# Kernel tuning notes

Hardware: AMD Instinct MI355X
Metric: run time of the kernel (lower is better)

## Reference

```python
import jax, jax.numpy as jnp
import numpy as np

N_NODES = 100
K = 8
EPS = 1e-8

def gru_last_hidden(x_seq, Wih, Whh, bih, bhh):
    # x_seq: [T, N, F]; torch GRU gate order: r, z, n
    xW = jnp.einsum('tnf,gf->tng', x_seq, Wih) + bih  # [T, N, 3H]
    H = Whh.shape[1]
    def step(h, xw):
        hW = h @ Whh.T + bhh
        xr, xz, xn = jnp.split(xw, 3, axis=-1)
        hr, hz, hn = jnp.split(hW, 3, axis=-1)
        r = jax.nn.sigmoid(xr + hr)
        z = jax.nn.sigmoid(xz + hz)
        n = jnp.tanh(xn + r * hn)
        h_new = (1.0 - z) * n + z * h
        return h_new, None
    h0 = jnp.zeros((x_seq.shape[1], H), x_seq.dtype)
    hT, _ = jax.lax.scan(step, h0, xW)
    return hT  # [N, H]

def knn_edges(emb, k):
    # cosine sim, zero diagonal, top-k neighbors per row
    nrm = jnp.linalg.norm(emb, axis=1, keepdims=True)
    a = emb / jnp.maximum(nrm, EPS)
    sim = a @ a.T
    idx = jnp.arange(sim.shape[0])
    sim = sim.at[idx, idx].set(0.0)
    _, tgt = jax.lax.top_k(sim, k)               # [N, k]
    src = jnp.broadcast_to(idx[:, None], tgt.shape)
    return src.reshape(-1), tgt.reshape(-1)      # each [N*k]

def sage_conv(x, src, tgt, Wl, Wr, b):
    # PyG SAGEConv (mean aggr): lin_l(mean of neighbor msgs) + lin_r(x) + b
    msg = x[src]                                  # [E, D]
    agg = jax.ops.segment_sum(msg, tgt, num_segments=x.shape[0])
    cnt = jax.ops.segment_sum(jnp.ones((src.shape[0],), x.dtype), tgt,
                              num_segments=x.shape[0])
    agg = agg / jnp.maximum(cnt, 1.0)[:, None]
    return agg @ Wl.T + x @ Wr.T + b

def setup_inputs() -> dict:
    key = jax.random.key(0)
    ks = jax.random.split(key, 16)
    T, N, F, H = 2048, N_NODES, 128, 512
    EMB, FLAT_IN, FLAT_OUT = 128, 32, 64
    GIN = H + FLAT_OUT + EMB       # 704
    GH, GOUT = 256, 128
    OUT_IN = GOUT + H              # 640
    s = 0.02
    return {
        'node_feat': jax.random.normal(ks[0], (T, N, F), jnp.float32),
        'flat': jax.random.normal(ks[1], (N, FLAT_IN), jnp.float32),
        'emb': jax.random.normal(ks[2], (N, EMB), jnp.float32) * s,
        'gru_Wih': jax.random.normal(ks[3], (3 * H, F), jnp.float32) * s,
        'gru_Whh': jax.random.normal(ks[4], (3 * H, H), jnp.float32) * s,
        'gru_bih': jnp.zeros((3 * H,), jnp.float32),
        'gru_bhh': jnp.zeros((3 * H,), jnp.float32),
        'flat_W': jax.random.normal(ks[5], (FLAT_OUT, FLAT_IN), jnp.float32) * s,
        'flat_b': jnp.zeros((FLAT_OUT,), jnp.float32),
        'sage1_Wl': jax.random.normal(ks[6], (GH, GIN), jnp.float32) * s,
        'sage1_Wr': jax.random.normal(ks[7], (GH, GIN), jnp.float32) * s,
        'sage1_b': jnp.zeros((GH,), jnp.float32),
        'sage2_Wl': jax.random.normal(ks[8], (GOUT, GH), jnp.float32) * s,
        'sage2_Wr': jax.random.normal(ks[9], (GOUT, GH), jnp.float32) * s,
        'sage2_b': jnp.zeros((GOUT,), jnp.float32),
        'out_W': jax.random.normal(ks[10], (1, OUT_IN), jnp.float32) * s,
        'out_b': jnp.zeros((1,), jnp.float32),
    }

def reference(node_feat, flat, emb, gru_Wih, gru_Whh, gru_bih, gru_bhh,
              flat_W, flat_b, sage1_Wl, sage1_Wr, sage1_b,
              sage2_Wl, sage2_Wr, sage2_b, out_W, out_b):
    # node_feat arrives [T, N, F]; torch code transposes to [N, T, F] for a
    # batch_first encoder, which equals time-major scan over [T, N, F] here.
    enc_out = gru_last_hidden(node_feat, gru_Wih, gru_Whh, gru_bih, gru_bhh)  # [N, H]
    flat_e = flat @ flat_W.T + flat_b                                          # [N, 64]
    gnn_in = jnp.concatenate([enc_out, flat_e, emb], axis=-1)                  # [N, 704]
    src, tgt = knn_edges(jax.lax.stop_gradient(emb), K)
    h = jax.nn.relu(sage_conv(gnn_in, src, tgt, sage1_Wl, sage1_Wr, sage1_b))
    g = sage_conv(h, src, tgt, sage2_Wl, sage2_Wr, sage2_b)                    # [N, 128]
    out_feat = jnp.concatenate([g, enc_out], axis=-1)                          # [N, 640]
    out = jax.nn.sigmoid(out_feat @ out_W.T + out_b)
    return out.squeeze(-1)                                                      # [N]
```

## Files before the change

kernel.cpp:

```cpp
#include <hip/hip_runtime.h>
#include <math.h>

#define TS   2048
#define NN   100
#define FD   128
#define HD   512
#define G3   1536
#define NG   7
#define NSL  8
#define KNN  8
#define GIN  704
#define GH   256
#define GOUT 128

typedef float  f32x4  __attribute__((ext_vector_type(4)));
typedef __bf16 bf16x8 __attribute__((ext_vector_type(8)));
#define MFMA16(a, b, c) __builtin_amdgcn_mfma_f32_16x16x32_bf16((a), (b), (c), 0, 0, 0)

#define WXST 136

__device__ __forceinline__ float sig_(float v) {
    return __builtin_amdgcn_rcpf(1.f + __expf(-v));
}
__device__ __forceinline__ float tanh_(float v) {
    float e = __expf(2.f * v);
    return 1.f - 2.f * __builtin_amdgcn_rcpf(e + 1.f);
}


#define GLD16_BODY(SC) \
        "global_load_dwordx4 %0, %16, %17" SC "\n\t" \
        "global_load_dwordx4 %1, %16, %17 offset:64" SC "\n\t" \
        "global_load_dwordx4 %2, %16, %17 offset:128" SC "\n\t" \
        "global_load_dwordx4 %3, %16, %17 offset:192" SC "\n\t" \
        "global_load_dwordx4 %4, %16, %17 offset:256" SC "\n\t" \
        "global_load_dwordx4 %5, %16, %17 offset:320" SC "\n\t" \
        "global_load_dwordx4 %6, %16, %17 offset:384" SC "\n\t" \
        "global_load_dwordx4 %7, %16, %17 offset:448" SC "\n\t" \
        "global_load_dwordx4 %8, %16, %17 offset:512" SC "\n\t" \
        "global_load_dwordx4 %9, %16, %17 offset:576" SC "\n\t" \
        "global_load_dwordx4 %10, %16, %17 offset:640" SC "\n\t" \
        "global_load_dwordx4 %11, %16, %17 offset:704" SC "\n\t" \
        "global_load_dwordx4 %12, %16, %17 offset:768" SC "\n\t" \
        "global_load_dwordx4 %13, %16, %17 offset:832" SC "\n\t" \
        "global_load_dwordx4 %14, %16, %17 offset:896" SC "\n\t" \
        "global_load_dwordx4 %15, %16, %17 offset:960" SC "\n\t" \
        "s_waitcnt vmcnt(0)"
#define GLD16_ARGS(h, voff, base) \
        : "=&v"(h[0]), "=&v"(h[1]), "=&v"(h[2]), "=&v"(h[3]), \
          "=&v"(h[4]), "=&v"(h[5]), "=&v"(h[6]), "=&v"(h[7]), \
          "=&v"(h[8]), "=&v"(h[9]), "=&v"(h[10]), "=&v"(h[11]), \
          "=&v"(h[12]), "=&v"(h[13]), "=&v"(h[14]), "=&v"(h[15]) \
        : "v"(voff), "s"(base) : "memory"

__device__ __forceinline__ void loadh16_l(const __bf16* base, unsigned voff, f32x4* h) {
    asm volatile(GLD16_BODY(" sc0") GLD16_ARGS(h, voff, base));
}
__device__ __forceinline__ void loadh16_a(const __bf16* base, unsigned voff, f32x4* h) {
    asm volatile(GLD16_BODY(" sc0 sc1") GLD16_ARGS(h, voff, base));
}

#define STH4_BODY(SC) \
        "global_store_short %4, %0, %5" SC "\n\t" \
        "global_store_short %4, %1, %5 offset:1024" SC "\n\t" \
        "global_store_short %4, %2, %5 offset:2048" SC "\n\t" \
        "global_store_short %4, %3, %5 offset:3072" SC
__device__ __forceinline__ void storeh4_l(__bf16* base, unsigned voff,
                                          unsigned v0, unsigned v1, unsigned v2, unsigned v3) {
    asm volatile(STH4_BODY(" sc0")
                 :: "v"(v0), "v"(v1), "v"(v2), "v"(v3), "v"(voff), "s"(base) : "memory");
}
__device__ __forceinline__ void storeh4_a(__bf16* base, unsigned voff,
                                          unsigned v0, unsigned v1, unsigned v2, unsigned v3) {
    asm volatile(STH4_BODY(" sc0 sc1")
                 :: "v"(v0), "v"(v1), "v"(v2), "v"(v3), "v"(voff), "s"(base) : "memory");
}

__device__ __forceinline__ void tagstore_l(int* base, unsigned voff, int val) {
    asm volatile("global_store_dword %1, %0, %2 sc0" :: "v"(val), "v"(voff), "s"(base) : "memory");
}
__device__ __forceinline__ void tagstore_a(int* base, unsigned voff, int val) {
    asm volatile("global_store_dword %1, %0, %2 sc0 sc1" :: "v"(val), "v"(voff), "s"(base) : "memory");
}
__device__ __forceinline__ int tagload_l(const int* base, unsigned voff) {
    int v;
    asm volatile("global_load_dword %0, %1, %2 sc0\n\ts_waitcnt vmcnt(0)"
                 : "=v"(v) : "v"(voff), "s"(base) : "memory");
    return v;
}
__device__ __forceinline__ int tagload_a(const int* base, unsigned voff) {
    int v;
    asm volatile("global_load_dword %0, %1, %2 sc0 sc1\n\ts_waitcnt vmcnt(0)"
                 : "=v"(v) : "v"(voff), "s"(base) : "memory");
    return v;
}

__device__ __forceinline__ bf16x8 cvt8(const float* p) {
    float4 a = *(const float4*)p, b = *(const float4*)(p + 4);
    bf16x8 r;
    r[0] = (__bf16)a.x; r[1] = (__bf16)a.y; r[2] = (__bf16)a.z; r[3] = (__bf16)a.w;
    r[4] = (__bf16)b.x; r[5] = (__bf16)b.y; r[6] = (__bf16)b.z; r[7] = (__bf16)b.w;
    return r;
}

template<bool LOCAL>
__device__ void gru_loop(const float* __restrict__ x,
                         const float* __restrict__ Wih, const float* __restrict__ Whh,
                         const float* __restrict__ bih, const float* __restrict__ bhh,
                         __bf16* h0buf, __bf16* h1buf, float* enc, int* tags,
                         int g, int s, __bf16* WxP, __bf16* AxP)
{
    const int tid = threadIdx.x;
    const int w   = tid >> 6;
    const int ln  = tid & 63;
    const int nb  = g * 16;
    const int mi  = ln & 15;
    const int kq8 = (ln >> 4) * 8;
    const int cl  = 16 * w + mi;
    const int ch  = 64 * s + cl;

    for (int idx = tid; idx < 192 * 32; idx += 256) {
        int row = idx >> 5, c4 = idx & 31;
        int grow = (row >> 6) * HD + 64 * s + (row & 63);
        float4 v = ((const float4*)(Wih + (size_t)grow * FD))[c4];
        __bf16* d = WxP + row * WXST + c4 * 4;
        d[0] = (__bf16)v.x; d[1] = (__bf16)v.y; d[2] = (__bf16)v.z; d[3] = (__bf16)v.w;
    }

    bf16x8 wR[16], wZ[16], wN[16];
    {
        const float* pR = Whh + (size_t)ch * HD;
        const float* pZ = Whh + (size_t)(HD + ch) * HD;
        const float* pN = Whh + (size_t)(2 * HD + ch) * HD;
        #pragma unroll
        for (int kk = 0; kk < 16; ++kk) {
            int ko = 32 * kk + kq8;
            wR[kk] = cvt8(pR + ko);
            wZ[kk] = cvt8(pZ + ko);
            wN[kk] = cvt8(pN + ko);
        }
    }
    const float bR  = bih[ch] + bhh[ch];
    const float bZ  = bih[HD + ch] + bhh[HD + ch];
    const float bNX = bih[2 * HD + ch];
    const float bNH = bhh[2 * HD + ch];

    const int xrow  = tid >> 4;
    const int xnode = nb + xrow;
    const int xcol  = (tid & 15) * 8;

    {
        float4 xa = {0.f, 0.f, 0.f, 0.f}, xb = xa;
        if (xnode < NN) {
            const float* xp = x + (size_t)xnode * FD + xcol;
            xa = ((const float4*)xp)[0];
            xb = ((const float4*)xp)[1];
        }
        bf16x8 v;
        v[0] = (__bf16)xa.x; v[1] = (__bf16)xa.y; v[2] = (__bf16)xa.z; v[3] = (__bf16)xa.w;
        v[4] = (__bf16)xb.x; v[5] = (__bf16)xb.y; v[6] = (__bf16)xb.z; v[7] = (__bf16)xb.w;
        *(bf16x8*)(AxP + (size_t)xrow * WXST + xcol) = v;
    }
    __syncthreads();

    f32x4 accR = {0.f, 0.f, 0.f, 0.f}, accZ = accR, accNX = accR, accNH = accR;
    #pragma unroll
    for (int kk = 0; kk < 4; ++kk) {
        int ko = 32 * kk + kq8;
        bf16x8 av = *(const bf16x8*)(AxP + (size_t)mi * WXST + ko);
        accR  = MFMA16(av, *(const bf16x8*)(WxP + (size_t)cl * WXST + ko),         accR);
        accZ  = MFMA16(av, *(const bf16x8*)(WxP + (size_t)(64 + cl) * WXST + ko),  accZ);
        accNX = MFMA16(av, *(const bf16x8*)(WxP + (size_t)(128 + cl) * WXST + ko), accNX);
    }

    float hold[4] = {0.f, 0.f, 0.f, 0.f};

    const unsigned hv_voff = ((unsigned)(nb + mi) * HD + (unsigned)kq8) * 2u;
    const unsigned st_voff = ((unsigned)(nb + (ln >> 4) * 4) * HD + (unsigned)ch) * 2u;
    const unsigned tg_self = (unsigned)(g * NSL + s) * 64u;
    const unsigned tg_poll = (unsigned)(g * NSL + (ln & 7)) * 64u;

    #pragma unroll 1
    for (int t = 0; t < TS; ++t) {
        __bf16* hcur = (t & 1) ? h1buf : h0buf;
        __bf16* hnxt = (t & 1) ? h0buf : h1buf;

        float4 xa = {0.f, 0.f, 0.f, 0.f}, xb = xa;
        if (t + 1 < TS && xnode < NN) {
            const float* xp = x + ((size_t)(t + 1) * NN + xnode) * FD + xcol;
            xa = ((const float4*)xp)[0];
            xb = ((const float4*)xp)[1];
        }

        for (;;) {
            int v = LOCAL ? tagload_l(tags, tg_poll) : tagload_a(tags, tg_poll);
            if (__all((ln < 8) ? (v >= t) : 1)) break;
        }

        f32x4 hv[16];
        if (LOCAL) loadh16_l(hcur, hv_voff, hv);
        else       loadh16_a(hcur, hv_voff, hv);

        #pragma unroll
        for (int kk = 0; kk < 16; ++kk) {
            bf16x8 av = __builtin_bit_cast(bf16x8, hv[kk]);
            accR  = MFMA16(av, wR[kk], accR);
            accZ  = MFMA16(av, wZ[kk], accZ);
            accNH = MFMA16(av, wN[kk], accNH);
        }

        unsigned pv[4];
        #pragma unroll
        for (int e = 0; e < 4; ++e) {
            float rv = sig_(accR[e] + bR);
            float zv = sig_(accZ[e] + bZ);
            float nv = tanh_(accNX[e] + bNX + rv * (accNH[e] + bNH));
            float hnew = (1.f - zv) * nv + zv * hold[e];
            hold[e] = hnew;
            pv[e] = (unsigned)__builtin_bit_cast(unsigned short, (__bf16)hnew);
        }
        if (LOCAL) storeh4_l(hnxt, st_voff, pv[0], pv[1], pv[2], pv[3]);
        else       storeh4_a(hnxt, st_voff, pv[0], pv[1], pv[2], pv[3]);
        asm volatile("s_waitcnt vmcnt(0)" ::: "memory");
        __syncthreads();
        if (tid == 0) {
            if (LOCAL) tagstore_l(tags, tg_self, t + 1);
            else       tagstore_a(tags, tg_self, t + 1);
        }

        const int nslot = (t + 1) & 1;
        if (t + 1 < TS) {
            bf16x8 v;
            v[0] = (__bf16)xa.x; v[1] = (__bf16)xa.y; v[2] = (__bf16)xa.z; v[3] = (__bf16)xa.w;
            v[4] = (__bf16)xb.x; v[5] = (__bf16)xb.y; v[6] = (__bf16)xb.z; v[7] = (__bf16)xb.w;
            *(bf16x8*)(AxP + ((size_t)nslot * 16 + xrow) * WXST + xcol) = v;
        }
        __syncthreads();

        accR = {0.f, 0.f, 0.f, 0.f}; accZ = accR; accNX = accR; accNH = accR;
        if (t + 1 < TS) {
            #pragma unroll
            for (int kk = 0; kk < 4; ++kk) {
                int ko = 32 * kk + kq8;
                bf16x8 av = *(const bf16x8*)(AxP + ((size_t)nslot * 16 + mi) * WXST + ko);
                accR  = MFMA16(av, *(const bf16x8*)(WxP + (size_t)cl * WXST + ko),         accR);
                accZ  = MFMA16(av, *(const bf16x8*)(WxP + (size_t)(64 + cl) * WXST + ko),  accZ);
                accNX = MFMA16(av, *(const bf16x8*)(WxP + (size_t)(128 + cl) * WXST + ko), accNX);
            }
        }
    }

    #pragma unroll
    for (int e = 0; e < 4; ++e) {
        int row = (ln >> 4) * 4 + e;
        if (nb + row < NN)
            enc[(size_t)(nb + row) * HD + ch] = hold[e];
    }
}

__global__ __launch_bounds__(256, 1) void gru_kernel(
    const float* __restrict__ x, const float* __restrict__ Wih,
    const float* __restrict__ Whh, const float* __restrict__ bih,
    const float* __restrict__ bhh,
    __bf16* h0buf, __bf16* h1buf, float* enc, int* sync)
{
    __shared__ int sh_slot, sh_loc;
    __shared__ __align__(16) __bf16 Wx[192 * WXST];
    __shared__ __align__(16) __bf16 Ax[2 * 16 * WXST];

    int* tags  = sync;
    int* claim = sync + 896;
    int* sxcc  = sync + 960;
    int* ready = sync + 1024;

    if (threadIdx.x == 0) {
        int xcc = 0;
        asm volatile("s_getreg_b32 %0, hwreg(HW_REG_XCC_ID)" : "=s"(xcc));
        int slot = -1;
        if (xcc < NG) {
            for (int k = xcc * NSL; k < xcc * NSL + NSL && slot < 0; ++k) {
                int e0 = 0;
                if (__hip_atomic_compare_exchange_strong(claim + k, &e0, 1,
                        __ATOMIC_RELAXED, __ATOMIC_RELAXED, __HIP_MEMORY_SCOPE_AGENT))
                    slot = k;
            }
        }
        for (int k = 0; k < NG * NSL && slot < 0; ++k) {
            int e0 = 0;
            if (__hip_atomic_compare_exchange_strong(claim + k, &e0, 1,
                    __ATOMIC_RELAXED, __ATOMIC_RELAXED, __HIP_MEMORY_SCOPE_AGENT))
                slot = k;
        }
        __hip_atomic_store(sxcc + slot, xcc + 1, __ATOMIC_RELAXED, __HIP_MEMORY_SCOPE_AGENT);
        __hip_atomic_fetch_add(ready, 1, __ATOMIC_RELAXED, __HIP_MEMORY_SCOPE_AGENT);
        while (__hip_atomic_load(ready, __ATOMIC_RELAXED, __HIP_MEMORY_SCOPE_AGENT) < NG * NSL)
            __builtin_amdgcn_s_sleep(8);
        int base = (slot / NSL) * NSL;
        int x0 = __hip_atomic_load(sxcc + base, __ATOMIC_RELAXED, __HIP_MEMORY_SCOPE_AGENT);
        int loc = 1;
        for (int k = 1; k < NSL; ++k)
            loc &= (__hip_atomic_load(sxcc + base + k, __ATOMIC_RELAXED,
                                      __HIP_MEMORY_SCOPE_AGENT) == x0);
        sh_slot = slot; sh_loc = loc;
    }
    __syncthreads();
    const int slot = sh_slot;
    const int g = slot / NSL, s = slot % NSL;

    if (sh_loc) gru_loop<true >(x, Wih, Whh, bih, bhh, h0buf, h1buf, enc, tags, g, s, Wx, Ax);
    else        gru_loop<false>(x, Wih, Whh, bih, bhh, h0buf, h1buf, enc, tags, g, s, Wx, Ax);
}


__global__ void e1_gnn_in(const float* __restrict__ enc, const float* __restrict__ flat,
                          const float* __restrict__ emb, const float* __restrict__ fW,
                          const float* __restrict__ fb, float* __restrict__ gnn)
{
    int i = blockIdx.x, tid = threadIdx.x;
    const float4* src = (const float4*)(enc + (size_t)i * HD);
    float4* dst = (float4*)(gnn + (size_t)i * GIN);
    dst[tid] = src[tid];
    if (tid < 64) {
        float acc = fb[tid];
        const float* w  = fW + tid * 32;
        const float* fl = flat + i * 32;
        #pragma unroll
        for (int k = 0; k < 32; ++k) acc = fmaf(fl[k], w[k], acc);
        gnn[(size_t)i * GIN + HD + tid] = acc;
    }
    gnn[(size_t)i * GIN + HD + 64 + tid] = emb[(size_t)i * FD + tid];
}

__global__ void e2a_norm(const float* __restrict__ emb, float* __restrict__ mx)
{
    int j = threadIdx.x;
    if (j < NN) {
        float acc = 0.f;
        const float* e = emb + (size_t)j * FD;
        for (int d = 0; d < FD; ++d) acc = fmaf(e[d], e[d], acc);
        mx[j] = fmaxf(sqrtf(acc), 1e-8f);
    }
}

__global__ void e2b_knn(const float* __restrict__ emb, const float* __restrict__ mx,
                        int* __restrict__ tgt)
{
    int i = blockIdx.x, tid = threadIdx.x;
    __shared__ float ei[FD];
    __shared__ float srow[NN];
    ei[tid] = emb[(size_t)i * FD + tid];
    __syncthreads();
    if (tid < NN) {
        float acc = 0.f;
        const float* e = emb + (size_t)tid * FD;
        for (int d = 0; d < FD; ++d) acc = fmaf(ei[d], e[d], acc);
        float sim = acc / (mx[i] * mx[tid]);
        srow[tid] = (tid == i) ? 0.f : sim;
    }
    __syncthreads();
    if (tid == 0) {
        for (int t = 0; t < KNN; ++t) {
            float best = -1e30f; int bi = 0;
            for (int j = 0; j < NN; ++j) { float v = srow[j]; if (v > best) { best = v; bi = j; } }
            srow[bi] = -1e30f;
            tgt[i * KNN + t] = bi;
        }
    }
}

__global__ void e3_agg(const float* __restrict__ xin, const int* __restrict__ tgt,
                       float* __restrict__ agg, float* __restrict__ cnt, int D)
{
    int e = blockIdx.x, src = e >> 3, tg = tgt[e];
    for (int d = threadIdx.x; d < D; d += blockDim.x)
        atomicAdd(&agg[(size_t)tg * D + d], xin[(size_t)src * D + d]);
    if (threadIdx.x == 0) atomicAdd(&cnt[tg], 1.0f);
}

__global__ void e4_sage(const float* __restrict__ agg, const float* __restrict__ xin,
                        const float* __restrict__ cnt,
                        const float* __restrict__ Wl, const float* __restrict__ Wr,
                        const float* __restrict__ b, float* __restrict__ out,
                        int Din, int Dout, int dorelu)
{
    int j = blockIdx.x, o = threadIdx.x;
    extern __shared__ float sm[];
    float* la = sm;
    float* lx = sm + Din;
    for (int d = o; d < Din; d += blockDim.x) {
        la[d] = agg[(size_t)j * Din + d];
        lx[d] = xin[(size_t)j * Din + d];
    }
    __syncthreads();
    float inv = 1.f / fmaxf(cnt[j], 1.f);
    float acc1 = 0.f, acc2 = 0.f;
    const float* wl = Wl + (size_t)o * Din;
    const float* wr = Wr + (size_t)o * Din;
    for (int k = 0; k < Din; ++k) {
        acc1 = fmaf(la[k], wl[k], acc1);
        acc2 = fmaf(lx[k], wr[k], acc2);
    }
    float v = fmaf(acc1, inv, acc2) + b[o];
    if (dorelu) v = fmaxf(v, 0.f);
    out[(size_t)j * Dout + o] = v;
}

__global__ void e7_out(const float* __restrict__ g, const float* __restrict__ enc,
                       const float* __restrict__ oW, const float* __restrict__ ob,
                       float* __restrict__ out)
{
    int j = threadIdx.x;
    if (j < NN) {
        float acc = ob[0];
        const float* gr = g + (size_t)j * GOUT;
        for (int d = 0; d < GOUT; ++d) acc = fmaf(gr[d], oW[d], acc);
        const float* er = enc + (size_t)j * HD;
        for (int d = 0; d < HD; ++d) acc = fmaf(er[d], oW[GOUT + d], acc);
        out[j] = 1.f / (1.f + expf(-acc));
    }
}

extern "C" void kernel_launch(void* const* d_in, const int* in_sizes, int n_in,
                              void* d_out, int out_size, void* d_ws, size_t ws_size,
                              hipStream_t stream)
{
    const float* x    = (const float*)d_in[0];
    const float* flat = (const float*)d_in[1];
    const float* emb  = (const float*)d_in[2];
    const float* Wih  = (const float*)d_in[3];
    const float* Whh  = (const float*)d_in[4];
    const float* bih  = (const float*)d_in[5];
    const float* bhh  = (const float*)d_in[6];
    const float* fW   = (const float*)d_in[7];
    const float* fb   = (const float*)d_in[8];
    const float* s1Wl = (const float*)d_in[9];
    const float* s1Wr = (const float*)d_in[10];
    const float* s1b  = (const float*)d_in[11];
    const float* s2Wl = (const float*)d_in[12];
    const float* s2Wr = (const float*)d_in[13];
    const float* s2b  = (const float*)d_in[14];
    const float* oW   = (const float*)d_in[15];
    const float* ob   = (const float*)d_in[16];
    float* out = (float*)d_out;

    char* p = (char*)d_ws;
    __bf16* h0buf = (__bf16*)(p + 0);
    float*  agg1  = (float*)(p + 114688);
    float*  agg2  = (float*)(p + 396288);
    float*  cnt1  = (float*)(p + 498688);
    float*  cnt2  = (float*)(p + 499136);
    int*    sync  = (int*)  (p + 499584);
    __bf16* h1buf = (__bf16*)(p + 504192);
    float*  enc   = (float*)(p + 618880);
    float*  gnn   = (float*)(p + 848256);
    float*  h1s   = (float*)(p + 1129856);
    float*  gbuf  = (float*)(p + 1232256);
    float*  mx    = (float*)(p + 1283456);
    int*    tgt   = (int*)  (p + 1283904);

    (void)hipMemsetAsync(d_ws, 0, 504192, stream);

    gru_kernel<<<NG * NSL, 256, 0, stream>>>(x, Wih, Whh, bih, bhh, h0buf, h1buf, enc, sync);
    e1_gnn_in<<<NN, 128, 0, stream>>>(enc, flat, emb, fW, fb, gnn);
    e2a_norm<<<1, 128, 0, stream>>>(emb, mx);
    e2b_knn<<<NN, 128, 0, stream>>>(emb, mx, tgt);
    e3_agg<<<NN * KNN, 256, 0, stream>>>(gnn, tgt, agg1, cnt1, GIN);
    e4_sage<<<NN, GH, 2 * GIN * sizeof(float), stream>>>(agg1, gnn, cnt1, s1Wl, s1Wr, s1b, h1s, GIN, GH, 1);
    e3_agg<<<NN * KNN, 256, 0, stream>>>(h1s, tgt, agg2, cnt2, GH);
    e4_sage<<<NN, GOUT, 2 * GH * sizeof(float), stream>>>(agg2, h1s, cnt2, s2Wl, s2Wr, s2b, gbuf, GH, GOUT, 0);
    e7_out<<<1, 128, 0, stream>>>(gbuf, enc, oW, ob, out);
}
```

Measured before the change: 8.504 ms.

## Drop XCC-local slot placement and split h-load wait into two halves

```diff
diff --git a/kernel.cpp b/kernel.cpp
--- a/kernel.cpp
+++ b/kernel.cpp
@@ -28,65 +28,49 @@
 }
 
 
-#define GLD16_BODY(SC) \
-        "global_load_dwordx4 %0, %16, %17" SC "\n\t" \
-        "global_load_dwordx4 %1, %16, %17 offset:64" SC "\n\t" \
-        "global_load_dwordx4 %2, %16, %17 offset:128" SC "\n\t" \
-        "global_load_dwordx4 %3, %16, %17 offset:192" SC "\n\t" \
-        "global_load_dwordx4 %4, %16, %17 offset:256" SC "\n\t" \
-        "global_load_dwordx4 %5, %16, %17 offset:320" SC "\n\t" \
-        "global_load_dwordx4 %6, %16, %17 offset:384" SC "\n\t" \
-        "global_load_dwordx4 %7, %16, %17 offset:448" SC "\n\t" \
-        "global_load_dwordx4 %8, %16, %17 offset:512" SC "\n\t" \
-        "global_load_dwordx4 %9, %16, %17 offset:576" SC "\n\t" \
-        "global_load_dwordx4 %10, %16, %17 offset:640" SC "\n\t" \
-        "global_load_dwordx4 %11, %16, %17 offset:704" SC "\n\t" \
-        "global_load_dwordx4 %12, %16, %17 offset:768" SC "\n\t" \
-        "global_load_dwordx4 %13, %16, %17 offset:832" SC "\n\t" \
-        "global_load_dwordx4 %14, %16, %17 offset:896" SC "\n\t" \
-        "global_load_dwordx4 %15, %16, %17 offset:960" SC "\n\t" \
+__device__ __forceinline__ void loadh8_lo(const __bf16* base, unsigned voff, f32x4* h) {
+    asm volatile(
+        "global_load_dwordx4 %0, %8, %9 sc0 sc1\n\t"
+        "global_load_dwordx4 %1, %8, %9 offset:64 sc0 sc1\n\t"
+        "global_load_dwordx4 %2, %8, %9 offset:128 sc0 sc1\n\t"
+        "global_load_dwordx4 %3, %8, %9 offset:192 sc0 sc1\n\t"
+        "global_load_dwordx4 %4, %8, %9 offset:256 sc0 sc1\n\t"
+        "global_load_dwordx4 %5, %8, %9 offset:320 sc0 sc1\n\t"
+        "global_load_dwordx4 %6, %8, %9 offset:384 sc0 sc1\n\t"
+        "global_load_dwordx4 %7, %8, %9 offset:448 sc0 sc1\n\t"
         "s_waitcnt vmcnt(0)"
-#define GLD16_ARGS(h, voff, base) \
-        : "=&v"(h[0]), "=&v"(h[1]), "=&v"(h[2]), "=&v"(h[3]), \
-          "=&v"(h[4]), "=&v"(h[5]), "=&v"(h[6]), "=&v"(h[7]), \
-          "=&v"(h[8]), "=&v"(h[9]), "=&v"(h[10]), "=&v"(h[11]), \
-          "=&v"(h[12]), "=&v"(h[13]), "=&v"(h[14]), "=&v"(h[15]) \
-        : "v"(voff), "s"(base) : "memory"
-
-__device__ __forceinline__ void loadh16_l(const __bf16* base, unsigned voff, f32x4* h) {
-    asm volatile(GLD16_BODY(" sc0") GLD16_ARGS(h, voff, base));
-}
-__device__ __forceinline__ void loadh16_a(const __bf16* base, unsigned voff, f32x4* h) {
-    asm volatile(GLD16_BODY(" sc0 sc1") GLD16_ARGS(h, voff, base));
-}
-
-#define STH4_BODY(SC) \
-        "global_store_short %4, %0, %5" SC "\n\t" \
-        "global_store_short %4, %1, %5 offset:1024" SC "\n\t" \
-        "global_store_short %4, %2, %5 offset:2048" SC "\n\t" \
-        "global_store_short %4, %3, %5 offset:3072" SC
-__device__ __forceinline__ void storeh4_l(__bf16* base, unsigned voff,
-                                          unsigned v0, unsigned v1, unsigned v2, unsigned v3) {
-    asm volatile(STH4_BODY(" sc0")
-                 :: "v"(v0), "v"(v1), "v"(v2), "v"(v3), "v"(voff), "s"(base) : "memory");
-}
+        : "=&v"(h[0]), "=&v"(h[1]), "=&v"(h[2]), "=&v"(h[3]),
+          "=&v"(h[4]), "=&v"(h[5]), "=&v"(h[6]), "=&v"(h[7])
+        : "v"(voff), "s"(base) : "memory");
+}
+__device__ __forceinline__ void loadh8_hi(const __bf16* base, unsigned voff, f32x4* h) {
+    asm volatile(
+        "global_load_dwordx4 %0, %8, %9 offset:512 sc0 sc1\n\t"
+        "global_load_dwordx4 %1, %8, %9 offset:576 sc0 sc1\n\t"
+        "global_load_dwordx4 %2, %8, %9 offset:640 sc0 sc1\n\t"
+        "global_load_dwordx4 %3, %8, %9 offset:704 sc0 sc1\n\t"
+        "global_load_dwordx4 %4, %8, %9 offset:768 sc0 sc1\n\t"
+        "global_load_dwordx4 %5, %8, %9 offset:832 sc0 sc1\n\t"
+        "global_load_dwordx4 %6, %8, %9 offset:896 sc0 sc1\n\t"
+        "global_load_dwordx4 %7, %8, %9 offset:960 sc0 sc1\n\t"
+        "s_waitcnt vmcnt(0)"
+        : "=&v"(h[0]), "=&v"(h[1]), "=&v"(h[2]), "=&v"(h[3]),
+          "=&v"(h[4]), "=&v"(h[5]), "=&v"(h[6]), "=&v"(h[7])
+        : "v"(voff), "s"(base) : "memory");
+}
+
 __device__ __forceinline__ void storeh4_a(__bf16* base, unsigned voff,
                                           unsigned v0, unsigned v1, unsigned v2, unsigned v3) {
-    asm volatile(STH4_BODY(" sc0 sc1")
-                 :: "v"(v0), "v"(v1), "v"(v2), "v"(v3), "v"(voff), "s"(base) : "memory");
-}
-
-__device__ __forceinline__ void tagstore_l(int* base, unsigned voff, int val) {
-    asm volatile("global_store_dword %1, %0, %2 sc0" :: "v"(val), "v"(voff), "s"(base) : "memory");
-}
+    asm volatile(
+        "global_store_short %4, %0, %5 sc0 sc1\n\t"
+        "global_store_short %4, %1, %5 offset:1024 sc0 sc1\n\t"
+        "global_store_short %4, %2, %5 offset:2048 sc0 sc1\n\t"
+        "global_store_short %4, %3, %5 offset:3072 sc0 sc1"
+        :: "v"(v0), "v"(v1), "v"(v2), "v"(v3), "v"(voff), "s"(base) : "memory");
+}
+
 __device__ __forceinline__ void tagstore_a(int* base, unsigned voff, int val) {
     asm volatile("global_store_dword %1, %0, %2 sc0 sc1" :: "v"(val), "v"(voff), "s"(base) : "memory");
-}
-__device__ __forceinline__ int tagload_l(const int* base, unsigned voff) {
-    int v;
-    asm volatile("global_load_dword %0, %1, %2 sc0\n\ts_waitcnt vmcnt(0)"
-                 : "=v"(v) : "v"(voff), "s"(base) : "memory");
-    return v;
 }
 __device__ __forceinline__ int tagload_a(const int* base, unsigned voff) {
     int v;
@@ -103,7 +87,6 @@
     return r;
 }
 
-template<bool LOCAL>
 __device__ void gru_loop(const float* __restrict__ x,
                          const float* __restrict__ Wih, const float* __restrict__ Whh,
                          const float* __restrict__ bih, const float* __restrict__ bhh,
@@ -192,21 +175,34 @@
             xb = ((const float4*)xp)[1];
         }
 
-        for (;;) {
-            int v = LOCAL ? tagload_l(tags, tg_poll) : tagload_a(tags, tg_poll);
-            if (__all((ln < 8) ? (v >= t) : 1)) break;
-        }
-
-        f32x4 hv[16];
-        if (LOCAL) loadh16_l(hcur, hv_voff, hv);
-        else       loadh16_a(hcur, hv_voff, hv);
-
+        unsigned rdy = 0;
+        do {
+            int v = tagload_a(tags, tg_poll);
+            rdy = (unsigned)(__ballot(v >= t) & 0xFFull);
+        } while ((rdy & 0x0Fu) != 0x0Fu);
+
+        f32x4 hv0[8];
+        loadh8_lo(hcur, hv_voff, hv0);
         #pragma unroll
-        for (int kk = 0; kk < 16; ++kk) {
-            bf16x8 av = __builtin_bit_cast(bf16x8, hv[kk]);
+        for (int kk = 0; kk < 8; ++kk) {
+            bf16x8 av = __builtin_bit_cast(bf16x8, hv0[kk]);
             accR  = MFMA16(av, wR[kk], accR);
             accZ  = MFMA16(av, wZ[kk], accZ);
             accNH = MFMA16(av, wN[kk], accNH);
+        }
+
+        while ((rdy & 0xF0u) != 0xF0u) {
+            int v = tagload_a(tags, tg_poll);
+            rdy = (unsigned)(__ballot(v >= t) & 0xFFull);
+        }
+        f32x4 hv1[8];
+        loadh8_hi(hcur, hv_voff, hv1);
+        #pragma unroll
+        for (int kk = 0; kk < 8; ++kk) {
+            bf16x8 av = __builtin_bit_cast(bf16x8, hv1[kk]);
+            accR  = MFMA16(av, wR[8 + kk], accR);
+            accZ  = MFMA16(av, wZ[8 + kk], accZ);
+            accNH = MFMA16(av, wN[8 + kk], accNH);
         }
 
         unsigned pv[4];
@@ -219,14 +215,10 @@
             hold[e] = hnew;
             pv[e] = (unsigned)__builtin_bit_cast(unsigned short, (__bf16)hnew);
         }
-        if (LOCAL) storeh4_l(hnxt, st_voff, pv[0], pv[1], pv[2], pv[3]);
-        else       storeh4_a(hnxt, st_voff, pv[0], pv[1], pv[2], pv[3]);
+        storeh4_a(hnxt, st_voff, pv[0], pv[1], pv[2], pv[3]);
         asm volatile("s_waitcnt vmcnt(0)" ::: "memory");
         __syncthreads();
-        if (tid == 0) {
-            if (LOCAL) tagstore_l(tags, tg_self, t + 1);
-            else       tagstore_a(tags, tg_self, t + 1);
-        }
+        if (tid == 0) tagstore_a(tags, tg_self, t + 1);
 
         const int nslot = (t + 1) & 1;
         if (t + 1 < TS) {
@@ -264,51 +256,13 @@
     const float* __restrict__ bhh,
     __bf16* h0buf, __bf16* h1buf, float* enc, int* sync)
 {
-    __shared__ int sh_slot, sh_loc;
     __shared__ __align__(16) __bf16 Wx[192 * WXST];
     __shared__ __align__(16) __bf16 Ax[2 * 16 * WXST];
 
-    int* tags  = sync;
-    int* claim = sync + 896;
-    int* sxcc  = sync + 960;
-    int* ready = sync + 1024;
-
-    if (threadIdx.x == 0) {
-        int xcc = 0;
-        asm volatile("s_getreg_b32 %0, hwreg(HW_REG_XCC_ID)" : "=s"(xcc));
-        int slot = -1;
-        if (xcc < NG) {
-            for (int k = xcc * NSL; k < xcc * NSL + NSL && slot < 0; ++k) {
-                int e0 = 0;
-                if (__hip_atomic_compare_exchange_strong(claim + k, &e0, 1,
-                        __ATOMIC_RELAXED, __ATOMIC_RELAXED, __HIP_MEMORY_SCOPE_AGENT))
-                    slot = k;
-            }
-        }
-        for (int k = 0; k < NG * NSL && slot < 0; ++k) {
-            int e0 = 0;
-            if (__hip_atomic_compare_exchange_strong(claim + k, &e0, 1,
-                    __ATOMIC_RELAXED, __ATOMIC_RELAXED, __HIP_MEMORY_SCOPE_AGENT))
-                slot = k;
-        }
-        __hip_atomic_store(sxcc + slot, xcc + 1, __ATOMIC_RELAXED, __HIP_MEMORY_SCOPE_AGENT);
-        __hip_atomic_fetch_add(ready, 1, __ATOMIC_RELAXED, __HIP_MEMORY_SCOPE_AGENT);
-        while (__hip_atomic_load(ready, __ATOMIC_RELAXED, __HIP_MEMORY_SCOPE_AGENT) < NG * NSL)
-            __builtin_amdgcn_s_sleep(8);
-        int base = (slot / NSL) * NSL;
-        int x0 = __hip_atomic_load(sxcc + base, __ATOMIC_RELAXED, __HIP_MEMORY_SCOPE_AGENT);
-        int loc = 1;
-        for (int k = 1; k < NSL; ++k)
-            loc &= (__hip_atomic_load(sxcc + base + k, __ATOMIC_RELAXED,
-                                      __HIP_MEMORY_SCOPE_AGENT) == x0);
-        sh_slot = slot; sh_loc = loc;
-    }
-    __syncthreads();
-    const int slot = sh_slot;
-    const int g = slot / NSL, s = slot % NSL;
-
-    if (sh_loc) gru_loop<true >(x, Wih, Whh, bih, bhh, h0buf, h1buf, enc, tags, g, s, Wx, Ax);
-    else        gru_loop<false>(x, Wih, Whh, bih, bhh, h0buf, h1buf, enc, tags, g, s, Wx, Ax);
+    const int g = blockIdx.x >> 3;
+    const int s = blockIdx.x & 7;
+
+    gru_loop(x, Wih, Whh, bih, bhh, h0buf, h1buf, enc, sync, g, s, Wx, Ax);
 }
 
 
```

After: 8.001 ms. 1.06x faster.
